# Performance work log

Measured on AMD Instinct MI355X. Metric: run time of the kernel, lower is better.

## Reference

```python
import jax, jax.numpy as jnp
import numpy as np

B, T, D = 32, 1024, 512   # batch, encoder length, listener feature dim (= speller hidden)
H = 512                   # speller_hidden_dim
V = 64                    # output_class_dim
S = 128                   # max_label_len (decode steps, no teacher forcing)


def setup_inputs() -> dict:
    key = jax.random.key(0)
    ks = jax.random.split(key, 7)
    s = lambda n: 1.0 / np.sqrt(n)
    return {
        "listener_feature": jax.random.normal(ks[0], (B, T, D), jnp.float32),
        "W_ih": jax.random.normal(ks[1], (4 * H, V + H), jnp.float32) * s(V + H),
        "W_hh": jax.random.normal(ks[2], (4 * H, H), jnp.float32) * s(H),
        "b_ih": jax.random.normal(ks[3], (4 * H,), jnp.float32) * 0.01,
        "b_hh": jax.random.normal(ks[4], (4 * H,), jnp.float32) * 0.01,
        "W_out": jax.random.normal(ks[5], (V, 2 * H), jnp.float32) * s(2 * H),
        "b_out": jax.random.normal(ks[6], (V,), jnp.float32) * 0.01,
    }


def reference(listener_feature, W_ih, W_hh, b_ih, b_hh, W_out, b_out):
    Bb = listener_feature.shape[0]

    def step(carry, _):
        h, c, x = carry                              # h,c: [B,H]; x: [B,V+H]
        gates = x @ W_ih.T + b_ih + h @ W_hh.T + b_hh  # [B,4H], torch gate order i,f,g,o
        i, f, g, o = jnp.split(gates, 4, axis=-1)
        i = jax.nn.sigmoid(i); f = jax.nn.sigmoid(f)
        g = jnp.tanh(g);       o = jax.nn.sigmoid(o)
        c = f * c + i * g
        h = o * jnp.tanh(c)                          # rnn_output [B,H]
        # dot attention over listener features
        energy = jnp.einsum('bd,btd->bt', h, listener_feature)   # [B,T]
        attn = jax.nn.softmax(energy, axis=-1)
        ctx = jnp.einsum('bt,btd->bd', attn, listener_feature)   # [B,D]
        concat = jnp.concatenate([h, ctx], axis=-1)              # [B,2H]
        logp = jax.nn.log_softmax(concat @ W_out.T + b_out, axis=-1)  # [B,V]
        # decode_mode == 1: greedy one-hot feedback (non-differentiable argmax)
        ow = jax.nn.one_hot(jnp.argmax(logp, axis=-1), V, dtype=logp.dtype)
        x_next = jnp.concatenate([ow, ctx], axis=-1)
        return (h, c, x_next), (logp, attn)

    # initial word = one-hot of class 0; first rnn input concatenates listener_feature[:,0,:]
    ow0 = jnp.zeros((Bb, V), listener_feature.dtype).at[:, 0].set(1.0)
    x0 = jnp.concatenate([ow0, listener_feature[:, 0, :]], axis=-1)
    h0 = jnp.zeros((Bb, H), listener_feature.dtype)
    c0 = jnp.zeros((Bb, H), listener_feature.dtype)

    _, (raw_pred_seq, attention_record) = jax.lax.scan(step, (h0, c0, x0), None, length=S)
    return raw_pred_seq, attention_record   # [S,B,V], [S,B,T]
```

## Files before the change

### kernel.cpp

```cpp
#include <hip/hip_runtime.h>

#define Bn 32
#define Tn 1024
#define Dn 512
#define Hn 512
#define Vn 64
#define Sn 128
#define NTS 8
#define TT 128
#define NTHREADS 512
#define KIH 576
#define NBLK 256

#define LDS_BYTES 143360
#define OUT_ATT ((size_t)Sn * Bn * Vn)

#define WS_XCTX  1024
#define WS_XH    17408
#define WS_LGP   50176
#define WS_MST   66560
#define WS_LST   66816
#define WS_CTXP  67072

struct F8 { float4 a, b; };

__device__ __forceinline__ float bfu(unsigned short u){ return __uint_as_float(((unsigned int)u)<<16); }
__device__ __forceinline__ float bflo(unsigned int u){ return __uint_as_float(u<<16); }
__device__ __forceinline__ float bfhi(unsigned int u){ return __uint_as_float(u & 0xffff0000u); }
__device__ __forceinline__ unsigned short f2bf(float f){
  unsigned int x = __float_as_uint(f);
  return (unsigned short)((x + 0x7fffu + ((x>>16)&1u)) >> 16);
}
__device__ __forceinline__ F8 ld8(const unsigned short* p){
  uint4 q = *(const uint4*)p;
  F8 r;
  r.a = make_float4(bflo(q.x), bfhi(q.x), bflo(q.y), bfhi(q.y));
  r.b = make_float4(bflo(q.z), bfhi(q.z), bflo(q.w), bfhi(q.w));
  return r;
}
__device__ __forceinline__ F8 ld8(const float* p){
  F8 r; r.a = *(const float4*)p; r.b = *(const float4*)(p+4); return r;
}
__device__ __forceinline__ float dot8(F8 w, float4 a, float4 b){
  return w.a.x*a.x + w.a.y*a.y + w.a.z*a.z + w.a.w*a.w
       + w.b.x*b.x + w.b.y*b.y + w.b.z*b.z + w.b.w*b.w;
}
__device__ __forceinline__ float dot64g(const unsigned short* __restrict__ w, const float* x){
  const float4* x4 = (const float4*)x;
  float acc = 0.f;
#pragma unroll
  for(int i=0;i<8;i++) acc += dot8(ld8(w+8*i), x4[2*i], x4[2*i+1]);
  return acc;
}
__device__ __forceinline__ float sigm(float x){
  x = fminf(fmaxf(x, -30.f), 30.f); return 1.f/(1.f + expf(-x));
}
__device__ __forceinline__ float tnh(float x){
  return tanhf(fminf(fmaxf(x, -20.f), 20.f));
}

template<int N>
__device__ __forceinline__ void rs_round(float* a, int off, bool hi){
#pragma unroll
  for(int i=0;i<N;i++){
    float send = hi ? a[i]   : a[i+N];
    float keep = hi ? a[i+N] : a[i];
    float recv = __shfl_xor(send, off);
    a[i] = keep + recv;
  }
}
__device__ __forceinline__ void rs32(float* a, int lane){
  rs_round<16>(a, 32, (lane&32)!=0);
  rs_round< 8>(a, 16, (lane&16)!=0);
  rs_round< 4>(a,  8, (lane& 8)!=0);
  rs_round< 2>(a,  4, (lane& 4)!=0);
  rs_round< 1>(a,  2, (lane& 2)!=0);
  a[0] += __shfl_xor(a[0], 1);
}

__device__ __forceinline__ void aput(float* p, float v){
  __hip_atomic_store(p, v, __ATOMIC_RELAXED, __HIP_MEMORY_SCOPE_AGENT);
}
__device__ __forceinline__ float aget(const float* p){
  return __hip_atomic_load(p, __ATOMIC_RELAXED, __HIP_MEMORY_SCOPE_AGENT);
}
__device__ __forceinline__ unsigned int uget(const unsigned int* p){
  return __hip_atomic_load(p, __ATOMIC_RELAXED, __HIP_MEMORY_SCOPE_AGENT);
}

__device__ __forceinline__ void gbar2(unsigned int* wsu, unsigned int ggen){
  asm volatile("s_waitcnt vmcnt(0)" ::: "memory");
  __syncthreads();
  const int tid = threadIdx.x;
  const int UP  = (int)blockIdx.x;
  const int grp = UP >> 3;
  if(UP == 0){
    if(tid < 64){
      if(tid == 0)
        __hip_atomic_fetch_add(&wsu[0], 1u, __ATOMIC_RELEASE, __HIP_MEMORY_SCOPE_AGENT);
      const unsigned int tgt = 8u*ggen;
      for(;;){
        unsigned int v = (tid < 32) ? uget(&wsu[tid*16]) : tgt;
        if(__all(v >= tgt)) break;
        __builtin_amdgcn_s_sleep(1);
      }
      if(tid < 32)
        __hip_atomic_store(&wsu[tid*16 + 8], ggen, __ATOMIC_RELEASE, __HIP_MEMORY_SCOPE_AGENT);
    }
  } else if(tid == 0){
    __hip_atomic_fetch_add(&wsu[grp*16], 1u, __ATOMIC_RELEASE, __HIP_MEMORY_SCOPE_AGENT);
    while(uget(&wsu[grp*16 + 8]) < ggen) __builtin_amdgcn_s_sleep(1);
  }
  if(tid == 0){
    unsigned int x = __hip_atomic_load(&wsu[grp*16 + 8], __ATOMIC_ACQUIRE, __HIP_MEMORY_SCOPE_AGENT);
    asm volatile("" :: "v"(x));
  }
  __syncthreads();
  asm volatile("" ::: "memory");
}

__device__ __forceinline__ void gbarE(unsigned int* line){
  asm volatile("s_waitcnt vmcnt(0)" ::: "memory");
  __syncthreads();
  if(threadIdx.x == 0){
    unsigned int g = uget(line+1);
    unsigned int p = __hip_atomic_fetch_add(line, 1u, __ATOMIC_RELEASE, __HIP_MEMORY_SCOPE_AGENT);
    if(p == g*8u + 7u){
      __hip_atomic_store(line+1, g+1u, __ATOMIC_RELEASE, __HIP_MEMORY_SCOPE_AGENT);
    } else {
      while(uget(line+1) == g) __builtin_amdgcn_s_sleep(1);
    }
    unsigned int x = __hip_atomic_load(line+1, __ATOMIC_ACQUIRE, __HIP_MEMORY_SCOPE_AGENT);
    asm volatile("" :: "v"(x));
  }
  __syncthreads();
  asm volatile("" ::: "memory");
}

__global__ void dtype_probe(const unsigned short* __restrict__ b3, unsigned int* flag){
  const int t = threadIdx.x;
  bool ok = true;
#pragma unroll
  for(int i=0;i<8;i++){
    float v = bfu(b3[2*(t*8+i)]);
    ok = ok && (v == v) && (fabsf(v) < 0.5f);
  }
  unsigned long long m = __ballot(ok);
  if(t == 0)
    __hip_atomic_store(flag, (m == ~0ull) ? 1u : 2u, __ATOMIC_RELEASE, __HIP_MEMORY_SCOPE_AGENT);
}

__global__ __launch_bounds__(NTHREADS, 1)
void speller_v3(const float* __restrict__ lf,  const float* __restrict__ wih,
                const float* __restrict__ whh, const float* __restrict__ bih,
                const float* __restrict__ bhh, const float* __restrict__ wout,
                const float* __restrict__ bout, float* __restrict__ out,
                float* __restrict__ ws)
{
  { unsigned int fl = __hip_atomic_load((unsigned int*)ws + 512, __ATOMIC_ACQUIRE, __HIP_MEMORY_SCOPE_AGENT);
    if(fl != 2u) return; }

  const int tid   = threadIdx.x;
  const int UP    = (int)blockIdx.x;
  const int b_att = UP >> 3;
  const int ts    = UP & 7;
  const int w     = tid >> 6;
  const int lane  = tid & 63;

  extern __shared__ char smem[];
  float* tile   = (float*)smem;
  float* epart  = (float*)(smem + 131072);
  float* h_s    = epart + 512;
  float* e_s    = h_s + 512;
  float* p_s    = e_s + 128;
  float* red_s  = p_s + 128;
  float* pre_s  = red_s + 32;
  float* ctxc_s = pre_s + 256;
  float* c_s    = ctxc_s + 64;
  float* bias_s = c_s + 64;
  float* bout_s = bias_s + 8;
  int*   pall_s = (int*)(bout_s + 64);
  float* wow_s  = (float*)(pall_s + 32);

  unsigned int* wsu   = (unsigned int*)ws;
  unsigned int* eline = wsu + (size_t)b_att*16 + 4;
  float* xctx = ws + WS_XCTX;
  float* xh   = ws + WS_XH;
  float* lgp  = ws + WS_LGP;
  float* mst  = ws + WS_MST;
  float* lst  = ws + WS_LST;
  float* ctxp = ws + WS_CTXP;

  const int rw = (w>>1)*Hn + 2*UP + (w&1);

  float4 wv0, wv1, wv2, wv3;
  {
    const int k0 = 16*lane;
    const float* wp = (lane < 32) ? (wih + (size_t)rw*KIH + 64 + k0)
                                  : (whh + (size_t)rw*Hn + (k0 - 512));
    wv0 = *(const float4*)wp;     wv1 = *(const float4*)(wp+4);
    wv2 = *(const float4*)(wp+8); wv3 = *(const float4*)(wp+12);
  }
  float4 oh0, oh1, oc0, oc1;
  {
    const int v = tid>>3, q = tid&7;
    const float* pH = wout + (size_t)v*(2*Hn) + ts*64 + q*8;
    const float* pC = pH + Hn;
    oh0 = *(const float4*)pH; oh1 = *(const float4*)(pH+4);
    oc0 = *(const float4*)pC; oc1 = *(const float4*)(pC+4);
  }

  {
    const int rr = tid>>6, cc = tid&63;
    const int r2 = (rr>>1)*Hn + 2*UP + (rr&1);
    wow_s[tid] = wih[(size_t)r2*KIH + cc];
  }
  if(tid < 8){ const int r2 = (tid>>1)*Hn + 2*UP + (tid&1); bias_s[tid] = bih[r2] + bhh[r2]; }
  if(tid < Vn) bout_s[tid] = bout[tid];
  if(tid < 64) c_s[tid] = 0.f;
  if(tid < 32) pall_s[tid] = 0;

  float lfreg[64];
  {
    const float4* s4 = (const float4*)(lf + ((size_t)b_att*Tn + (size_t)ts*TT) * Dn);
    float4* d4 = (float4*)tile;
#pragma unroll
    for(int i=0;i<16;i++){
      const int f = tid + i*NTHREADS;
      const int row = f >> 7, cc = f & 127;
      d4[(row << 7) | (cc ^ (row & 7))] = s4[f];
    }
    const float* lfg = lf + ((size_t)b_att*Tn + (size_t)ts*TT + 64) * Dn + tid;
#pragma unroll
    for(int j=0;j<64;j++) lfreg[j] = lfg[(size_t)j*Dn];
  }

  if(tid < 64){
    aput(&xctx[(size_t)b_att*Dn + ts*64 + tid], lf[(size_t)b_att*Tn*Dn + ts*64 + tid]);
    const int bb = tid>>1, ul = tid&1;
    aput(&xh[(size_t)Bn*Hn + (size_t)bb*Hn + 2*UP + ul], 0.f);
  }
  __syncthreads();
  unsigned int gg = 0;
  gbar2(wsu, ++gg);

  for(int s = 0; s <= Sn; ++s){
    if(s > 0){
      for(int ii=0; ii<4; ++ii){
        const int bb = 4*w + ii;
        float lv = bout_s[lane];
        const float4* lp = (const float4*)(lgp + ((size_t)bb*Vn + lane)*8);
        float4 qa = lp[0], qb = lp[1];
        lv += qa.x+qa.y+qa.z+qa.w + qb.x+qb.y+qb.z+qb.w;
        float mv = lv; int mi = lane;
#pragma unroll
        for(int off=1; off<64; off<<=1){
          float ov = __shfl_xor(mv, off);
          int   oi = __shfl_xor(mi, off);
          if(ov > mv || (ov == mv && oi < mi)){ mv = ov; mi = oi; }
        }
        float se = expf(lv - mv);
#pragma unroll
        for(int off=1; off<64; off<<=1) se += __shfl_xor(se, off);
        if(lane == 0) pall_s[bb] = mi;
        if(UP == 8*bb) out[((size_t)(s-1)*Bn + bb)*Vn + lane] = lv - mv - logf(se);
      }
    }
    if(s == Sn) break;
    __syncthreads();

    {
      const float* xhR = xh + (size_t)(((s+1)&1))*Bn*Hn;
      const int k0 = 16*lane;
      const float* xbase = (lane < 32) ? (xctx + k0) : (xhR + (k0 - 512));
      float acc[Bn];
#pragma unroll
      for(int bb=0; bb<Bn; ++bb){
        const float4* xp = (const float4*)(xbase + (size_t)bb*Dn);
        float4 x0 = xp[0], x1 = xp[1], x2 = xp[2], x3 = xp[3];
        acc[bb] = wv0.x*x0.x + wv0.y*x0.y + wv0.z*x0.z + wv0.w*x0.w
                + wv1.x*x1.x + wv1.y*x1.y + wv1.z*x1.z + wv1.w*x1.w
                + wv2.x*x2.x + wv2.y*x2.y + wv2.z*x2.z + wv2.w*x2.w
                + wv3.x*x3.x + wv3.y*x3.y + wv3.z*x3.z + wv3.w*x3.w;
      }
      rs32(acc, lane);
      if((lane & 1) == 0) pre_s[w*Bn + (lane>>1)] = acc[0];
    }
    __syncthreads();
    if(tid < 64){
      const int bb = tid>>1, ul = tid&1;
      const int pidx = pall_s[bb];
      float gi = sigm(pre_s[(0+ul)*Bn+bb] + wow_s[(0+ul)*64+pidx] + bias_s[0+ul]);
      float gf = sigm(pre_s[(2+ul)*Bn+bb] + wow_s[(2+ul)*64+pidx] + bias_s[2+ul]);
      float gg2 = tnh(pre_s[(4+ul)*Bn+bb] + wow_s[(4+ul)*64+pidx] + bias_s[4+ul]);
      float go = sigm(pre_s[(6+ul)*Bn+bb] + wow_s[(6+ul)*64+pidx] + bias_s[6+ul]);
      float c = gf*c_s[tid] + gi*gg2;
      c_s[tid] = c;
      aput(&xh[(size_t)(s&1)*Bn*Hn + (size_t)bb*Hn + 2*UP + ul], go*tnh(c));
    }
    gbar2(wsu, ++gg);

    h_s[tid] = xh[(size_t)(s&1)*Bn*Hn + (size_t)b_att*Hn + tid];
    __syncthreads();
    {
      const int t1 = tid >> 3, q = tid & 7, mm = t1 & 7;
      const float4* lrow = (const float4*)tile + (size_t)t1*128;
      const float4* hq = (const float4*)(h_s + q*64);
      float ea = 0.f;
#pragma unroll
      for(int i=0;i<8;i++){
        const int c0 = q*16 + 2*i;
        F8 wv; wv.a = lrow[c0 ^ mm]; wv.b = lrow[(c0+1) ^ mm];
        ea += dot8(wv, hq[2*i], hq[2*i+1]);
      }
#pragma unroll
      for(int off=1; off<8; off<<=1) ea += __shfl_xor(ea, off);
      if(q==0) e_s[t1] = ea;
    }
    {
      const float h_own = h_s[tid];
      float a[32];
#pragma unroll
      for(int j=0;j<32;j++) a[j] = h_own * lfreg[j];
      rs32(a, lane);
      if((lane & 1) == 0) epart[(w<<6) + (lane>>1)] = a[0];
#pragma unroll
      for(int j=0;j<32;j++) a[j] = h_own * lfreg[32+j];
      rs32(a, lane);
      if((lane & 1) == 0) epart[(w<<6) + 32 + (lane>>1)] = a[0];
    }
    __syncthreads();
    if(tid < 64){
      float s2 = 0.f;
#pragma unroll
      for(int w2=0; w2<8; w2++) s2 += epart[(w2<<6) + tid];
      e_s[64 + tid] = s2;
      float v = fmaxf(e_s[tid], s2);
#pragma unroll
      for(int off=1; off<64; off<<=1) v = fmaxf(v, __shfl_xor(v,off));
      if(tid==0) red_s[10] = v;
    }
    __syncthreads();
    if(tid < TT) p_s[tid] = expf(e_s[tid] - red_s[10]);
    __syncthreads();
    if(tid < 64){
      float v = p_s[tid] + p_s[tid+64];
#pragma unroll
      for(int off=1; off<64; off<<=1) v += __shfl_xor(v,off);
      if(tid==0){
        aput(&mst[(size_t)b_att*NTS + ts], red_s[10]);
        aput(&lst[(size_t)b_att*NTS + ts], v);
      }
    }
    {
      float acc = 0.f;
      const int cs = tid >> 2, cr = tid & 3;
#pragma unroll
      for(int t=0;t<64;t++)
        acc += p_s[t] * tile[(size_t)t*Dn + (((cs ^ (t&7))<<2) | cr)];
#pragma unroll
      for(int j=0;j<64;j++) acc += p_s[64+j] * lfreg[j];
      aput(&ctxp[((size_t)b_att*NTS + ts)*Dn + tid], acc);
    }
    gbarE(eline);

    if(tid < NTS){
      red_s[16+tid] = mst[(size_t)b_att*NTS + tid];
      red_s[24+tid] = lst[(size_t)b_att*NTS + tid];
    }
    __syncthreads();
    if(tid == 0){
      float m = -3.0e38f;
#pragma unroll
      for(int j=0;j<NTS;j++) m = fmaxf(m, red_s[16+j]);
      float l = 0.f;
#pragma unroll
      for(int j=0;j<NTS;j++){ float fac = expf(red_s[16+j]-m); red_s[j]=fac; l += fac*red_s[24+j]; }
      red_s[8]=m; red_s[9]=l;
    }
    __syncthreads();
    {
      const float gm = red_s[8];
      const float gl = red_s[9];
      if(tid < TT)
        out[OUT_ATT + ((size_t)s*Bn + b_att)*Tn + (size_t)ts*TT + tid] = expf(e_s[tid] - gm)/gl;
      if(tid < 64){
        const int d = ts*64 + tid;
        float acc = 0.f;
#pragma unroll
        for(int j=0;j<NTS;j++) acc += red_s[j] * ctxp[((size_t)b_att*NTS + j)*Dn + d];
        const float cv = acc / gl;
        ctxc_s[tid] = cv;
        aput(&xctx[(size_t)b_att*Dn + d], cv);
      }
    }
    __syncthreads();
    {
      const int v = tid>>3, q = tid&7;
      const float4* hp = (const float4*)(h_s + ts*64 + q*8);
      const float4* cp = (const float4*)(ctxc_s + q*8);
      float4 ha = hp[0], hb = hp[1], ca = cp[0], cb = cp[1];
      float acc = oh0.x*ha.x + oh0.y*ha.y + oh0.z*ha.z + oh0.w*ha.w
                + oh1.x*hb.x + oh1.y*hb.y + oh1.z*hb.z + oh1.w*hb.w
                + oc0.x*ca.x + oc0.y*ca.y + oc0.z*ca.z + oc0.w*ca.w
                + oc1.x*cb.x + oc1.y*cb.y + oc1.z*cb.z + oc1.w*cb.w;
#pragma unroll
      for(int off=1; off<8; off<<=1) acc += __shfl_xor(acc, off);
      if(q == 0) aput(&lgp[((size_t)b_att*Vn + v)*8 + ts], acc);
    }
    gbar2(wsu, ++gg);
  }
}

__device__ __forceinline__ void gbar8(unsigned int* bar){
  asm volatile("s_waitcnt vmcnt(0)" ::: "memory");
  __syncthreads();
  if(threadIdx.x==0){
    unsigned int g = uget(bar+1);
    unsigned int p = __hip_atomic_fetch_add(bar, 1u, __ATOMIC_RELAXED, __HIP_MEMORY_SCOPE_AGENT);
    if(p == g*NTS + (NTS-1)){
      __hip_atomic_store(bar+1, g+1u, __ATOMIC_RELAXED, __HIP_MEMORY_SCOPE_AGENT);
    } else {
      while(uget(bar+1) == g) __builtin_amdgcn_s_sleep(2);
    }
  }
  __syncthreads();
  asm volatile("" ::: "memory");
}

__global__ __launch_bounds__(NTHREADS, 2)
void speller_bf16(const unsigned short* __restrict__ lf, const unsigned short* __restrict__ wih,
                  const unsigned short* __restrict__ whh, const unsigned short* __restrict__ bih,
                  const unsigned short* __restrict__ bhh, const unsigned short* __restrict__ wout,
                  const unsigned short* __restrict__ bout, unsigned short* __restrict__ out,
                  float* __restrict__ ws)
{
  { unsigned int fl = __hip_atomic_load((unsigned int*)ws + 512, __ATOMIC_ACQUIRE, __HIP_MEMORY_SCOPE_AGENT);
    if(fl != 1u) return; }
  const int tid = threadIdx.x;
  const int b   = (int)(blockIdx.x >> 3);
  const int ts  = (int)(blockIdx.x & 7);

  extern __shared__ char smem[];
  unsigned short* lf_s = (unsigned short*)smem;
  float* h_s   = (float*)(smem + 131072);
  float* ctx_s = h_s + 512;
  float* e_s   = ctx_s + 512;
  float* p_s   = e_s + 128;
  float* lg_s  = p_s + 128;
  float* red_s = lg_s + 64;
  float* c_s   = red_s + 32;
  int*   i_s   = (int*)(c_s + 64);

  unsigned int* bar = (unsigned int*)ws + (size_t)b*16 + 4;
  float* hbuf = ws + 1024  + (size_t)b*Hn;
  float* mstB = ws + WS_MST + (size_t)b*NTS;
  float* lstB = ws + WS_LST + (size_t)b*NTS;
  float* ctxpB= ws + WS_CTXP + (size_t)b*NTS*Dn;

  {
    const uint4* s4 = (const uint4*)(lf + ((size_t)b*Tn + (size_t)ts*TT) * Dn);
    uint4* d4 = (uint4*)lf_s;
#pragma unroll
    for(int i=0;i<16;i++) d4[tid + i*NTHREADS] = s4[tid + i*NTHREADS];
  }
  h_s[tid] = 0.f;
  if(tid < 64) c_s[tid] = 0.f;
  if(tid == 0) i_s[0] = 0;
  __syncthreads();

  for(int s = 0; s <= Sn; ++s){
    if(s > 0){
      if(tid < NTS){ red_s[16+tid] = aget(&mstB[tid]); red_s[24+tid] = aget(&lstB[tid]); }
      __syncthreads();
      if(tid == 0){
        float m = -3.0e38f;
#pragma unroll
        for(int j=0;j<NTS;j++) m = fmaxf(m, red_s[16+j]);
        float l = 0.f;
#pragma unroll
        for(int j=0;j<NTS;j++){ float fac = expf(red_s[16+j]-m); red_s[j]=fac; l += fac*red_s[24+j]; }
        red_s[8]=m; red_s[9]=l;
      }
      __syncthreads();
      const float gm = red_s[8];
      const float gl = red_s[9];
      {
        float acc = 0.f;
#pragma unroll
        for(int j=0;j<NTS;j++) acc += red_s[j] * aget(&ctxpB[(size_t)j*Dn + tid]);
        ctx_s[tid] = acc / gl;
      }
      if(tid < TT)
        out[OUT_ATT + ((size_t)(s-1)*Bn + b)*Tn + (size_t)ts*TT + tid] = f2bf(expf(e_s[tid]-gm)/gl);
      __syncthreads();
      {
        const int j = tid >> 3, ks = tid & 7;
        const unsigned short* wr = wout + (size_t)j*(2*Hn) + ks*128;
        float acc;
        if(ks < 4) acc = dot64g(wr, h_s + ks*128)       + dot64g(wr+64, h_s + ks*128 + 64);
        else       acc = dot64g(wr, ctx_s + (ks-4)*128) + dot64g(wr+64, ctx_s + (ks-4)*128 + 64);
#pragma unroll
        for(int off=1; off<8; off<<=1) acc += __shfl_xor(acc, off);
        if(ks==0) lg_s[j] = acc + bfu(bout[j]);
      }
      __syncthreads();
      if(tid < Vn){
        const float lv = lg_s[tid];
        float mv = lv; int mi = tid;
#pragma unroll
        for(int off=1; off<64; off<<=1){
          float ov = __shfl_xor(mv, off);
          int   oi = __shfl_xor(mi, off);
          if(ov > mv || (ov == mv && oi < mi)){ mv = ov; mi = oi; }
        }
        float se = expf(lv - mv);
#pragma unroll
        for(int off=1; off<64; off<<=1) se += __shfl_xor(se, off);
        if(ts == 0) out[((size_t)(s-1)*Bn + b)*Vn + tid] = f2bf(lv - mv - logf(se));
        if(tid == 0) i_s[0] = mi;
      }
      __syncthreads();
    } else {
      ctx_s[tid] = bfu(lf[(size_t)b*Tn*Dn + tid]);
      __syncthreads();
    }

    if(s == Sn) break;

    {
      const int u  = tid >> 3;
      const int ks = tid & 7;
      const int uu = ts*64 + u;
      const unsigned short* wi0 = wih + (size_t)(       uu)*KIH + 64 + ks*64;
      const unsigned short* wi1 = wih + (size_t)(  Hn + uu)*KIH + 64 + ks*64;
      const unsigned short* wi2 = wih + (size_t)(2*Hn + uu)*KIH + 64 + ks*64;
      const unsigned short* wi3 = wih + (size_t)(3*Hn + uu)*KIH + 64 + ks*64;
      const unsigned short* wh0 = whh + (size_t)(       uu)*Hn + ks*64;
      const unsigned short* wh1 = whh + (size_t)(  Hn + uu)*Hn + ks*64;
      const unsigned short* wh2 = whh + (size_t)(2*Hn + uu)*Hn + ks*64;
      const unsigned short* wh3 = whh + (size_t)(3*Hn + uu)*Hn + ks*64;
      const float4* xc = (const float4*)(ctx_s + ks*64);
      const float4* xh4 = (const float4*)(h_s   + ks*64);
      float a0=0.f,a1=0.f,a2=0.f,a3=0.f;
#pragma unroll
      for(int i=0;i<8;i++){
        float4 p0 = xc[2*i], p1 = xc[2*i+1];
        a0 += dot8(ld8(wi0+8*i), p0, p1);
        a1 += dot8(ld8(wi1+8*i), p0, p1);
        a2 += dot8(ld8(wi2+8*i), p0, p1);
        a3 += dot8(ld8(wi3+8*i), p0, p1);
      }
#pragma unroll
      for(int i=0;i<8;i++){
        float4 p0 = xh4[2*i], p1 = xh4[2*i+1];
        a0 += dot8(ld8(wh0+8*i), p0, p1);
        a1 += dot8(ld8(wh1+8*i), p0, p1);
        a2 += dot8(ld8(wh2+8*i), p0, p1);
        a3 += dot8(ld8(wh3+8*i), p0, p1);
      }
#pragma unroll
      for(int off=1; off<8; off<<=1){
        a0 += __shfl_xor(a0, off);
        a1 += __shfl_xor(a1, off);
        a2 += __shfl_xor(a2, off);
        a3 += __shfl_xor(a3, off);
      }
      if(ks == 0){
        const int pidx = i_s[0];
        const int r0 = uu, r1 = Hn+uu, r2 = 2*Hn+uu, r3 = 3*Hn+uu;
        float gi = a0 + bfu(wih[(size_t)r0*KIH + pidx]) + bfu(bih[r0]) + bfu(bhh[r0]);
        float gf = a1 + bfu(wih[(size_t)r1*KIH + pidx]) + bfu(bih[r1]) + bfu(bhh[r1]);
        float gg = a2 + bfu(wih[(size_t)r2*KIH + pidx]) + bfu(bih[r2]) + bfu(bhh[r2]);
        float go = a3 + bfu(wih[(size_t)r3*KIH + pidx]) + bfu(bih[r3]) + bfu(bhh[r3]);
        gi = sigm(gi); gf = sigm(gf); gg = tnh(gg); go = sigm(go);
        float c = gf*c_s[u] + gi*gg;
        c_s[u] = c;
        aput(&hbuf[uu], go * tnh(c));
      }
    }
    gbar8(bar);

    h_s[tid] = aget(&hbuf[tid]);
    __syncthreads();
    {
      const int t2 = tid >> 3;
      const int q  = tid & 7;
      const float4* hq = (const float4*)(h_s + q*64);
      float ea=0.f, eb=0.f;
      const unsigned short* la = lf_s + (size_t)(2*t2  )*Dn + q*64;
      const unsigned short* lb = lf_s + (size_t)(2*t2+1)*Dn + q*64;
#pragma unroll
      for(int i=0;i<8;i++){
        float4 p0 = hq[2*i], p1 = hq[2*i+1];
        ea += dot8(ld8(la+8*i), p0, p1);
        eb += dot8(ld8(lb+8*i), p0, p1);
      }
#pragma unroll
      for(int off=1; off<8; off<<=1){ ea += __shfl_xor(ea,off); eb += __shfl_xor(eb,off); }
      if(q==0){ e_s[2*t2] = ea; e_s[2*t2+1] = eb; }
    }
    __syncthreads();
    if(tid < 64){
      float v = fmaxf(e_s[tid], e_s[tid+64]);
#pragma unroll
      for(int off=1; off<64; off<<=1) v = fmaxf(v, __shfl_xor(v,off));
      if(tid==0) red_s[10] = v;
    }
    __syncthreads();
    if(tid < TT) p_s[tid] = expf(e_s[tid] - red_s[10]);
    __syncthreads();
    if(tid < 64){
      float v = p_s[tid] + p_s[tid+64];
#pragma unroll
      for(int off=1; off<64; off<<=1) v += __shfl_xor(v,off);
      if(tid==0){ aput(&mstB[ts], red_s[10]); aput(&lstB[ts], v); }
    }
    {
      float acc = 0.f;
      const unsigned short* col = lf_s + tid;
#pragma unroll 4
      for(int t=0;t<TT;t++) acc += p_s[t] * bfu(col[(size_t)t*Dn]);
      aput(&ctxpB[(size_t)ts*Dn + tid], acc);
    }
    gbar8(bar);
  }
}

extern "C" void kernel_launch(void* const* d_in, const int* in_sizes, int n_in,
                              void* d_out, int out_size, void* d_ws, size_t ws_size,
                              hipStream_t stream) {
  (void)in_sizes; (void)n_in; (void)out_size; (void)ws_size;
  float* ws = (float*)d_ws;

  hipFuncSetAttribute(reinterpret_cast<const void*>(&speller_v3),
                      hipFuncAttributeMaxDynamicSharedMemorySize, LDS_BYTES);
  hipFuncSetAttribute(reinterpret_cast<const void*>(&speller_bf16),
                      hipFuncAttributeMaxDynamicSharedMemorySize, LDS_BYTES);
  hipMemsetAsync(d_ws, 0, 4096, stream);
  dtype_probe<<<dim3(1), dim3(64), 0, stream>>>((const unsigned short*)d_in[3],
                                                (unsigned int*)d_ws + 512);
  speller_v3<<<dim3(NBLK), dim3(NTHREADS), LDS_BYTES, stream>>>(
      (const float*)d_in[0], (const float*)d_in[1], (const float*)d_in[2],
      (const float*)d_in[3], (const float*)d_in[4], (const float*)d_in[5],
      (const float*)d_in[6], (float*)d_out, ws);
  speller_bf16<<<dim3(NBLK), dim3(NTHREADS), LDS_BYTES, stream>>>(
      (const unsigned short*)d_in[0], (const unsigned short*)d_in[1],
      (const unsigned short*)d_in[2], (const unsigned short*)d_in[3],
      (const unsigned short*)d_in[4], (const unsigned short*)d_in[5],
      (const unsigned short*)d_in[6], (unsigned short*)d_out, ws);
}
```

Baseline: 6.769 ms.

## Tile LSTM gate matvec by 8 units x 8 batches per block; decentralize grid barrier

Each block previously computed 2 hidden units for all 32 batch rows. It now computes 8 units for an 8-row batch group, holding 4 weight rows per wave in registers so each loaded input vector feeds four rows, which cuts the global reads of x/h per block. The grid barrier changes from a master block that gathers arrivals and broadcasts a release flag to every block polling all 32 group counters directly. That removes a release hop but puts more polling traffic on those counter lines, and the larger weight footprint raises register and LDS use.

```diff
diff --git a/kernel.cpp b/kernel.cpp
--- a/kernel.cpp
+++ b/kernel.cpp
@@ -12,7 +12,7 @@
 #define KIH 576
 #define NBLK 256
 
-#define LDS_BYTES 143360
+#define LDS_BYTES 147456
 #define OUT_ATT ((size_t)Sn * Bn * Vn)
 
 #define WS_XCTX  1024
@@ -92,28 +92,20 @@
   asm volatile("s_waitcnt vmcnt(0)" ::: "memory");
   __syncthreads();
   const int tid = threadIdx.x;
-  const int UP  = (int)blockIdx.x;
-  const int grp = UP >> 3;
-  if(UP == 0){
-    if(tid < 64){
-      if(tid == 0)
-        __hip_atomic_fetch_add(&wsu[0], 1u, __ATOMIC_RELEASE, __HIP_MEMORY_SCOPE_AGENT);
-      const unsigned int tgt = 8u*ggen;
-      for(;;){
-        unsigned int v = (tid < 32) ? uget(&wsu[tid*16]) : tgt;
-        if(__all(v >= tgt)) break;
-        __builtin_amdgcn_s_sleep(1);
-      }
-      if(tid < 32)
-        __hip_atomic_store(&wsu[tid*16 + 8], ggen, __ATOMIC_RELEASE, __HIP_MEMORY_SCOPE_AGENT);
-    }
-  } else if(tid == 0){
+  const int grp = (int)blockIdx.x >> 3;
+  if(tid == 0)
     __hip_atomic_fetch_add(&wsu[grp*16], 1u, __ATOMIC_RELEASE, __HIP_MEMORY_SCOPE_AGENT);
-    while(uget(&wsu[grp*16 + 8]) < ggen) __builtin_amdgcn_s_sleep(1);
-  }
-  if(tid == 0){
-    unsigned int x = __hip_atomic_load(&wsu[grp*16 + 8], __ATOMIC_ACQUIRE, __HIP_MEMORY_SCOPE_AGENT);
-    asm volatile("" :: "v"(x));
+  if(tid < 64){
+    const unsigned int tgt = 8u*ggen;
+    for(;;){
+      unsigned int v = (tid < 32) ? uget(&wsu[tid*16]) : tgt;
+      if(__all(v >= tgt)) break;
+      __builtin_amdgcn_s_sleep(1);
+    }
+    if(tid == 0){
+      unsigned int x = __hip_atomic_load(&wsu[grp*16], __ATOMIC_ACQUIRE, __HIP_MEMORY_SCOPE_AGENT);
+      asm volatile("" :: "v"(x));
+    }
   }
   __syncthreads();
   asm volatile("" ::: "memory");
@@ -164,6 +156,8 @@
   const int UP    = (int)blockIdx.x;
   const int b_att = UP >> 3;
   const int ts    = UP & 7;
+  const int ug    = UP >> 2;
+  const int bg    = UP & 3;
   const int w     = tid >> 6;
   const int lane  = tid & 63;
 
@@ -178,7 +172,7 @@
   float* ctxc_s = pre_s + 256;
   float* c_s    = ctxc_s + 64;
   float* bias_s = c_s + 64;
-  float* bout_s = bias_s + 8;
+  float* bout_s = bias_s + 32;
   int*   pall_s = (int*)(bout_s + 64);
   float* wow_s  = (float*)(pall_s + 32);
 
@@ -191,15 +185,19 @@
   float* lst  = ws + WS_LST;
   float* ctxp = ws + WS_CTXP;
 
-  const int rw = (w>>1)*Hn + 2*UP + (w&1);
-
-  float4 wv0, wv1, wv2, wv3;
+  float4 wv[4][4];
   {
-    const int k0 = 16*lane;
-    const float* wp = (lane < 32) ? (wih + (size_t)rw*KIH + 64 + k0)
-                                  : (whh + (size_t)rw*Hn + (k0 - 512));
-    wv0 = *(const float4*)wp;     wv1 = *(const float4*)(wp+4);
-    wv2 = *(const float4*)(wp+8); wv3 = *(const float4*)(wp+12);
+#pragma unroll
+    for(int r=0;r<4;++r){
+      const int row_loc = 4*w + r;
+      const int grow = (row_loc>>3)*Hn + ug*8 + (row_loc&7);
+      const float* wp = (lane < 32) ? (wih + (size_t)grow*KIH + 64 + 16*lane)
+                                    : (whh + (size_t)grow*Hn + (16*lane - 512));
+      wv[r][0] = ((const float4*)wp)[0];
+      wv[r][1] = ((const float4*)wp)[1];
+      wv[r][2] = ((const float4*)wp)[2];
+      wv[r][3] = ((const float4*)wp)[3];
+    }
   }
   float4 oh0, oh1, oc0, oc1;
   {
@@ -210,12 +208,17 @@
     oc0 = *(const float4*)pC; oc1 = *(const float4*)(pC+4);
   }
 
-  {
-    const int rr = tid>>6, cc = tid&63;
-    const int r2 = (rr>>1)*Hn + 2*UP + (rr&1);
-    wow_s[tid] = wih[(size_t)r2*KIH + cc];
-  }
-  if(tid < 8){ const int r2 = (tid>>1)*Hn + 2*UP + (tid&1); bias_s[tid] = bih[r2] + bhh[r2]; }
+#pragma unroll
+  for(int i=0;i<4;i++){
+    const int idx = tid + i*NTHREADS;
+    const int row_loc = idx >> 6, cc = idx & 63;
+    const int grow = (row_loc>>3)*Hn + ug*8 + (row_loc&7);
+    wow_s[idx] = wih[(size_t)grow*KIH + cc];
+  }
+  if(tid < 32){
+    const int grow = (tid>>3)*Hn + ug*8 + (tid&7);
+    bias_s[tid] = bih[grow] + bhh[grow];
+  }
   if(tid < Vn) bout_s[tid] = bout[tid];
   if(tid < 64) c_s[tid] = 0.f;
   if(tid < 32) pall_s[tid] = 0;
@@ -237,8 +240,8 @@
 
   if(tid < 64){
     aput(&xctx[(size_t)b_att*Dn + ts*64 + tid], lf[(size_t)b_att*Tn*Dn + ts*64 + tid]);
-    const int bb = tid>>1, ul = tid&1;
-    aput(&xh[(size_t)Bn*Hn + (size_t)bb*Hn + 2*UP + ul], 0.f);
+    const int bb = bg*8 + (tid>>3), u = ug*8 + (tid&7);
+    aput(&xh[(size_t)Bn*Hn + (size_t)bb*Hn + u], 0.f);
   }
   __syncthreads();
   unsigned int gg = 0;
@@ -272,31 +275,39 @@
     {
       const float* xhR = xh + (size_t)(((s+1)&1))*Bn*Hn;
       const int k0 = 16*lane;
-      const float* xbase = (lane < 32) ? (xctx + k0) : (xhR + (k0 - 512));
-      float acc[Bn];
-#pragma unroll
-      for(int bb=0; bb<Bn; ++bb){
-        const float4* xp = (const float4*)(xbase + (size_t)bb*Dn);
+      const float* xbase = (lane < 32) ? (xctx + (size_t)(bg*8)*Dn + k0)
+                                       : (xhR  + (size_t)(bg*8)*Hn + (k0 - 512));
+      float acc[32];
+#pragma unroll
+      for(int bb=0; bb<8; ++bb){
+        const float4* xp = (const float4*)(xbase + (size_t)bb*512);
         float4 x0 = xp[0], x1 = xp[1], x2 = xp[2], x3 = xp[3];
-        acc[bb] = wv0.x*x0.x + wv0.y*x0.y + wv0.z*x0.z + wv0.w*x0.w
-                + wv1.x*x1.x + wv1.y*x1.y + wv1.z*x1.z + wv1.w*x1.w
-                + wv2.x*x2.x + wv2.y*x2.y + wv2.z*x2.z + wv2.w*x2.w
-                + wv3.x*x3.x + wv3.y*x3.y + wv3.z*x3.z + wv3.w*x3.w;
+#pragma unroll
+        for(int r=0;r<4;++r){
+          acc[r*8+bb] = wv[r][0].x*x0.x + wv[r][0].y*x0.y + wv[r][0].z*x0.z + wv[r][0].w*x0.w
+                      + wv[r][1].x*x1.x + wv[r][1].y*x1.y + wv[r][1].z*x1.z + wv[r][1].w*x1.w
+                      + wv[r][2].x*x2.x + wv[r][2].y*x2.y + wv[r][2].z*x2.z + wv[r][2].w*x2.w
+                      + wv[r][3].x*x3.x + wv[r][3].y*x3.y + wv[r][3].z*x3.z + wv[r][3].w*x3.w;
+        }
       }
       rs32(acc, lane);
-      if((lane & 1) == 0) pre_s[w*Bn + (lane>>1)] = acc[0];
+      if((lane & 1) == 0){
+        const int i = lane>>1;
+        pre_s[(w*4 + (i>>3))*8 + (i&7)] = acc[0];
+      }
     }
     __syncthreads();
     if(tid < 64){
-      const int bb = tid>>1, ul = tid&1;
+      const int bb_loc = tid>>3, u_loc = tid&7;
+      const int bb = bg*8 + bb_loc;
       const int pidx = pall_s[bb];
-      float gi = sigm(pre_s[(0+ul)*Bn+bb] + wow_s[(0+ul)*64+pidx] + bias_s[0+ul]);
-      float gf = sigm(pre_s[(2+ul)*Bn+bb] + wow_s[(2+ul)*64+pidx] + bias_s[2+ul]);
-      float gg2 = tnh(pre_s[(4+ul)*Bn+bb] + wow_s[(4+ul)*64+pidx] + bias_s[4+ul]);
-      float go = sigm(pre_s[(6+ul)*Bn+bb] + wow_s[(6+ul)*64+pidx] + bias_s[6+ul]);
+      float gi = sigm(pre_s[(0*8+u_loc)*8+bb_loc] + wow_s[(0*8+u_loc)*64+pidx] + bias_s[0*8+u_loc]);
+      float gf = sigm(pre_s[(1*8+u_loc)*8+bb_loc] + wow_s[(1*8+u_loc)*64+pidx] + bias_s[1*8+u_loc]);
+      float gg2 = tnh(pre_s[(2*8+u_loc)*8+bb_loc] + wow_s[(2*8+u_loc)*64+pidx] + bias_s[2*8+u_loc]);
+      float go = sigm(pre_s[(3*8+u_loc)*8+bb_loc] + wow_s[(3*8+u_loc)*64+pidx] + bias_s[3*8+u_loc]);
       float c = gf*c_s[tid] + gi*gg2;
       c_s[tid] = c;
-      aput(&xh[(size_t)(s&1)*Bn*Hn + (size_t)bb*Hn + 2*UP + ul], go*tnh(c));
+      aput(&xh[(size_t)(s&1)*Bn*Hn + (size_t)bb*Hn + ug*8 + u_loc], go*tnh(c));
     }
     gbar2(wsu, ++gg);
 
@@ -310,8 +321,8 @@
 #pragma unroll
       for(int i=0;i<8;i++){
         const int c0 = q*16 + 2*i;
-        F8 wv; wv.a = lrow[c0 ^ mm]; wv.b = lrow[(c0+1) ^ mm];
-        ea += dot8(wv, hq[2*i], hq[2*i+1]);
+        F8 wvv; wvv.a = lrow[c0 ^ mm]; wvv.b = lrow[(c0+1) ^ mm];
+        ea += dot8(wvv, hq[2*i], hq[2*i+1]);
       }
 #pragma unroll
       for(int off=1; off<8; off<<=1) ea += __shfl_xor(ea, off);
```

Result: slower. 7.119 ms (+5.2%).
